# Optimization experiments

Measured on AMD Instinct MI355X. Metric: run time of the kernel, lower is better.

Reference implementation:

```python
import jax, jax.numpy as jnp
import numpy as np
import math

LMAX = 2
NUM_Z = 4
N_NODES = 20000
N_GRAPHS = 5000
N_EDGES = 320000
# irreps as (mul, l, parity)
IR_SH   = [(1, 0, 1), (1, 1, -1), (1, 2, 1)]
IR_ATTR = [(NUM_Z**2, 0, 1), (NUM_Z**2, 1, -1), (NUM_Z**2, 2, 1)]
IR_MID  = [(64, 0, 1), (24, 1, 1), (24, 1, -1), (16, 2, 1), (16, 2, -1)]
IR_OUT  = [(1, 0, -1), (6, 0, 1)]


def _cg(j1, j2, j3, m1, m2, m3):
    if m1 + m2 != m3:
        return 0.0
    f = math.factorial
    pre = math.sqrt((2 * j3 + 1) * f(j3 + j1 - j2) * f(j3 - j1 + j2) * f(j1 + j2 - j3) / f(j1 + j2 + j3 + 1))
    pre *= math.sqrt(f(j3 + m3) * f(j3 - m3) * f(j1 - m1) * f(j1 + m1) * f(j2 - m2) * f(j2 + m2))
    s = 0.0
    for k in range(max(0, j2 - j3 - m1, j1 - j3 + m2), min(j1 + j2 - j3, j1 - m1, j2 + m2) + 1):
        s += (-1) ** k / (f(k) * f(j1 + j2 - j3 - k) * f(j1 - m1 - k) * f(j2 + m2 - k) * f(j3 - j2 + m1 + k) * f(j3 - j1 - m2 + k))
    return pre * s


def _u(l):
    # complex -> real spherical harmonics change of basis, m = -l..l
    U = np.zeros((2 * l + 1, 2 * l + 1), dtype=complex)
    for m in range(-l, l + 1):
        if m > 0:
            U[m + l, -m + l] = 1 / math.sqrt(2)
            U[m + l, m + l] = (-1) ** m / math.sqrt(2)
        elif m == 0:
            U[l, l] = 1.0
        else:
            U[m + l, m + l] = 1j / math.sqrt(2)
            U[m + l, -m + l] = -1j * (-1) ** (-m) / math.sqrt(2)
    return U


def _w3j(l1, l2, l3):
    C = np.zeros((2 * l1 + 1, 2 * l2 + 1, 2 * l3 + 1))
    for m1 in range(-l1, l1 + 1):
        for m2 in range(-l2, l2 + 1):
            m3 = m1 + m2
            if -l3 <= m3 <= l3:
                C[m1 + l1, m2 + l2, m3 + l3] = _cg(l1, l2, l3, m1, m2, m3)
    T = np.einsum('am,bn,co,mno->abc', _u(l1), _u(l2), _u(l3).conj(), C.astype(complex))
    T = T.real if np.abs(T.real).max() >= np.abs(T.imag).max() else T.imag
    return (T / np.linalg.norm(T)).astype(np.float32)  # Frobenius norm 1, e3nn convention


W3J = {(a, b, c): _w3j(a, b, c) for a in range(3) for b in range(3) for c in range(3) if abs(a - b) <= c <= a + b}


def _slices(ir):
    s = [0]
    for m, l, _ in ir:
        s.append(s[-1] + m * (2 * l + 1))
    return s


def _paths(ir1, ir2, iro):
    paths = []
    fan = [0] * len(iro)
    off = 0
    for a, (m1, l1, p1) in enumerate(ir1):
        for b, (m2, l2, p2) in enumerate(ir2):
            for c, (m3, l3, p3) in enumerate(iro):
                if p1 * p2 == p3 and abs(l1 - l2) <= l3 <= l1 + l2:
                    paths.append((a, b, c, off))
                    fan[c] += m1 * m2
                    off += m1 * m2 * m3
    return paths, fan, off


def _fctp(x1, x2, w, ir1, ir2, iro):
    # FullyConnectedTensorProduct: 'uvw' weighted Clebsch-Gordan contraction per path
    s1, s2 = _slices(ir1), _slices(ir2)
    paths, fan, _ = _paths(ir1, ir2, iro)
    E = x1.shape[0]
    out = [jnp.zeros((E, m * (2 * l + 1)), x1.dtype) for m, l, _ in iro]
    for a, b, c, off in paths:
        m1, l1, _ = ir1[a]
        m2, l2, _ = ir2[b]
        m3, l3, _ = iro[c]
        W = w[off:off + m1 * m2 * m3].reshape(m1, m2, m3)
        C = jnp.asarray(W3J[(l1, l2, l3)], x1.dtype)
        xa = x1[:, s1[a]:s1[a + 1]].reshape(E, m1, 2 * l1 + 1)
        xb = x2[:, s2[b]:s2[b + 1]].reshape(E, m2, 2 * l2 + 1)
        alpha = math.sqrt(2 * l3 + 1) / math.sqrt(fan[c])
        y = jnp.einsum('eui,evj,ijk,uvw->ewk', xa, xb, C, W)
        out[c] = out[c] + (alpha * y).reshape(E, -1)
    return jnp.concatenate(out, axis=1)


def _sh(v):
    # component-normalized harmonic polynomials for l=0,1,2 (normalize=False)
    x, y, z = v[:, 0], v[:, 1], v[:, 2]
    r2 = x * x + y * y + z * z
    s3, s15, s5 = math.sqrt(3.0), math.sqrt(15.0), math.sqrt(5.0)
    sh1 = s3 * jnp.stack([y, z, x], axis=1)
    sh2 = jnp.stack([s15 * x * y, s15 * y * z, 0.5 * s5 * (3 * z * z - r2), s15 * x * z, 0.5 * s15 * (x * x - y * y)], axis=1)
    return jnp.concatenate([jnp.ones_like(x)[:, None], sh1, sh2], axis=1)  # [E, 9]


def _forward(pos, w_tp1, w_tp2, z, batch, edge_src, edge_dst):
    E = edge_src.shape[0]
    ev = pos[edge_src] - pos[edge_dst]
    sh = _sh(ev)
    zz = NUM_Z * z[edge_src] + z[edge_dst]
    zzf = jax.nn.one_hot(zz, NUM_Z ** 2, dtype=sh.dtype) * NUM_Z  # [E, 16]
    # 'uvu' TensorProduct of (16x0e) with sh: outer product per l block
    blocks = [(0, 1), (1, 4), (4, 9)]
    edge_attr = jnp.concatenate([(zzf[:, :, None] * sh[:, None, a:b]).reshape(E, -1) for a, b in blocks], axis=1)
    inv_nn = 1.0 / math.sqrt(3.0)  # num_neighbors = 3
    node = jax.ops.segment_sum(sh, edge_dst, num_segments=N_NODES) * inv_nn
    ef = _fctp(node[edge_src], edge_attr, w_tp1, IR_SH, IR_ATTR, IR_MID)
    node = jax.ops.segment_sum(ef, edge_dst, num_segments=N_NODES) * inv_nn
    ef = _fctp(node[edge_src], edge_attr, w_tp2, IR_MID, IR_ATTR, IR_OUT)
    node = jax.ops.segment_sum(ef, edge_dst, num_segments=N_NODES) * inv_nn
    return jax.ops.segment_sum(node, batch, num_segments=N_GRAPHS) * 0.5  # num_nodes = 4


def setup_inputs() -> dict:
    key = jax.random.key(0)
    k = jax.random.split(key, 7)
    _, _, n1 = _paths(IR_SH, IR_ATTR, IR_MID)
    _, _, n2 = _paths(IR_MID, IR_ATTR, IR_OUT)
    return {
        'pos': jax.random.normal(k[0], (N_NODES, 3), jnp.float32),
        'z': jax.random.randint(k[1], (N_NODES,), 0, NUM_Z, jnp.int32),
        'batch': jnp.sort(jax.random.randint(k[2], (N_NODES,), 0, N_GRAPHS, jnp.int32)),
        'edge_src': jax.random.randint(k[3], (N_EDGES,), 0, N_NODES, jnp.int32),
        'edge_dst': jax.random.randint(k[4], (N_EDGES,), 0, N_NODES, jnp.int32),
        'w_tp1': jax.random.normal(k[5], (n1,), jnp.float32),
        'w_tp2': jax.random.normal(k[6], (n2,), jnp.float32),
    }


def reference(pos, z, batch, edge_src, edge_dst, w_tp1, w_tp2):
    return _forward(pos, w_tp1, w_tp2, z, batch, edge_src, edge_dst)
```

## Files before the change

kernel.cpp:

```cpp
#include <hip/hip_runtime.h>


#define N_EDGES   320000
#define NN_NODES  20000
#define NN_GRAPHS 5000

__device__ __forceinline__ void sh_from_vec(float x, float y, float z,
                                            float* B1, float* B2) {
    const float s3   = 1.7320508075688772f;
    const float s15  = 3.8729833462074170f;
    const float s5h  = 1.1180339887498949f;
    const float s15h = 1.9364916731037085f;
    B1[0] = s3 * y; B1[1] = s3 * z; B1[2] = s3 * x;
    float r2 = x * x + y * y + z * z;
    B2[0] = s15 * x * y;
    B2[1] = s15 * y * z;
    B2[2] = s5h * (3.f * z * z - r2);
    B2[3] = s15 * x * z;
    B2[4] = s15h * (x * x - y * y);
}

__global__ __launch_bounds__(256) void k_zero(const float* __restrict__ pos,
                                              int* __restrict__ counts,
                                              float* __restrict__ out,
                                              float4* __restrict__ pos4) {
    int tid = blockIdx.x * blockDim.x + threadIdx.x;
    int stride = gridDim.x * blockDim.x;
    for (int i = tid; i < NN_NODES; i += stride) counts[i] = 0;
    for (int i = tid; i < NN_GRAPHS * 7; i += stride) out[i] = 0.f;
    for (int i = tid; i < NN_NODES; i += stride) {
        float4 p;
        p.x = pos[3 * i]; p.y = pos[3 * i + 1]; p.z = pos[3 * i + 2]; p.w = 0.f;
        pos4[i] = p;
    }
}

__global__ __launch_bounds__(256) void k_hist(const int* __restrict__ edst,
                                              int* __restrict__ counts) {
    int e = blockIdx.x * blockDim.x + threadIdx.x;
    if (e < N_EDGES) atomicAdd(&counts[edst[e]], 1);
}

__global__ __launch_bounds__(1024) void k_scan(const int* __restrict__ counts,
                                               int* __restrict__ start,
                                               int* __restrict__ cursor) {
    __shared__ int sdata[1024];
    __shared__ int carry;
    int tid = threadIdx.x;
    if (tid == 0) carry = 0;
    __syncthreads();
    for (int base = 0; base < NN_NODES; base += 1024) {
        int i = base + tid;
        int v = (i < NN_NODES) ? counts[i] : 0;
        sdata[tid] = v;
        __syncthreads();
        for (int off = 1; off < 1024; off <<= 1) {
            int t = (tid >= off) ? sdata[tid - off] : 0;
            __syncthreads();
            sdata[tid] += t;
            __syncthreads();
        }
        int incl = sdata[tid];
        int c = carry;
        if (i < NN_NODES) {
            int excl = c + incl - v;
            start[i] = excl;
            cursor[i] = excl;
        }
        __syncthreads();
        if (tid == 0) carry = c + sdata[1023];
        __syncthreads();
    }
    if (tid == 0) start[NN_NODES] = carry;
}

__global__ __launch_bounds__(256) void k_fill(const int* __restrict__ esrc,
                                              const int* __restrict__ edst,
                                              const int* __restrict__ zarr,
                                              int* __restrict__ cursor,
                                              int* __restrict__ csr) {
    int e = blockIdx.x * blockDim.x + threadIdx.x;
    if (e >= N_EDGES) return;
    int d = edst[e];
    int s = esrc[e];
    int q = 4 * zarr[s] + zarr[d];
    int p = atomicAdd(&cursor[d], 1);
    csr[p] = s | (q << 16) | ((d & 7) << 20);
}

__global__ __launch_bounds__(256) void k_nodesh(const float4* __restrict__ pos4,
                                                const int* __restrict__ start,
                                                const int* __restrict__ csr,
                                                float* __restrict__ node_sh) {
    int wave = threadIdx.x >> 6;
    int lane = threadIdx.x & 63;
    int n = blockIdx.x * 4 + wave;
    if (n >= NN_NODES) return;
    float4 pd = pos4[n];
    int s0 = start[n], s1 = start[n + 1];
    float acc[9] = {0.f, 0.f, 0.f, 0.f, 0.f, 0.f, 0.f, 0.f, 0.f};
    for (int idx = s0 + lane; idx < s1; idx += 64) {
        int s = csr[idx] & 0xFFFF;
        float4 ps = pos4[s];
        float x = ps.x - pd.x;
        float y = ps.y - pd.y;
        float z = ps.z - pd.z;
        float B1[3], B2[5];
        sh_from_vec(x, y, z, B1, B2);
        acc[0] += 1.f;
        acc[1] += B1[0]; acc[2] += B1[1]; acc[3] += B1[2];
        acc[4] += B2[0]; acc[5] += B2[1]; acc[6] += B2[2];
        acc[7] += B2[3]; acc[8] += B2[4];
    }
#pragma unroll
    for (int off = 32; off > 0; off >>= 1)
#pragma unroll
        for (int i = 0; i < 9; i++) acc[i] += __shfl_down(acc[i], off, 64);
    if (lane == 0) {
        const float inv_nn = 0.57735026918962576f;
#pragma unroll
        for (int i = 0; i < 9; i++) node_sh[n * 12 + i] = acc[i] * inv_nn;
    }
}

__global__ __launch_bounds__(512, 6) void k_mid(const float4* __restrict__ pos4,
                                                const float* __restrict__ node_sh,
                                                const int* __restrict__ start,
                                                const int* __restrict__ csr,
                                                const float* __restrict__ w1,
                                                float* __restrict__ mid) {
    __shared__ float Gl[8 * 816];
    int t = threadIdx.x;
    for (int i = t; i < 8 * 816; i += 512) Gl[i] = 0.f;
    __syncthreads();

    int nbase = blockIdx.x * 8;
    int e0 = start[nbase], e1 = start[nbase + 8];

    const float r3  = 0.57735026918962576f;
    const float r5  = 0.44721359549995794f;
    const float r6  = 0.40824829046386302f;
    const float r10 = 0.31622776601683794f;
    const float s30 = 0.18257418583505536f;
    const float rt3 = 1.7320508075688772f;
    const float c222 = 0.58554004376911990f;
    const float q6 = 0.40824829046386302f;
    const float h6 = 0.20412414523193151f;
    const float h2 = 0.35355339059327376f;
    const float r2c = 0.70710678118654752f;

    for (int idx = e0 + t; idx < e1; idx += 512) {
        int pk = csr[idx];
        int s = pk & 0xFFFF;
        int q = (pk >> 16) & 15;
        int r = (pk >> 20) & 7;
        float4 pd = pos4[nbase + r];
        float4 ps = pos4[s];
        float x = ps.x - pd.x;
        float y = ps.y - pd.y;
        float z = ps.z - pd.z;
        float B1[3], B2[5];
        sh_from_vec(x, y, z, B1, B2);
        const float4 nv0 = *(const float4*)(node_sh + s * 12);
        const float4 nv1 = *(const float4*)(node_sh + s * 12 + 4);
        float a0 = nv0.x;
        float A1[3] = {nv0.y, nv0.z, nv0.w};
        float A2[5] = {nv1.x, nv1.y, nv1.z, nv1.w, node_sh[s * 12 + 8]};
        float* gr = Gl + r * 816 + q * 51;

        atomicAdd(gr + 0, a0);
        atomicAdd(gr + 1, a0 * B1[0] * r3);
        atomicAdd(gr + 2, a0 * B1[1] * r3);
        atomicAdd(gr + 3, a0 * B1[2] * r3);
        atomicAdd(gr + 4, a0 * B2[0] * r5);
        atomicAdd(gr + 5, a0 * B2[1] * r5);
        atomicAdd(gr + 6, a0 * B2[2] * r5);
        atomicAdd(gr + 7, a0 * B2[3] * r5);
        atomicAdd(gr + 8, a0 * B2[4] * r5);
        atomicAdd(gr + 9,  A1[0] * r3);
        atomicAdd(gr + 10, A1[1] * r3);
        atomicAdd(gr + 11, A1[2] * r3);
        atomicAdd(gr + 12, -r3 * (A1[0] * B1[0] + A1[1] * B1[1] + A1[2] * B1[2]));
        atomicAdd(gr + 13, -r6 * (A1[1] * B1[2] - A1[2] * B1[1]));
        atomicAdd(gr + 14, -r6 * (A1[2] * B1[0] - A1[0] * B1[2]));
        atomicAdd(gr + 15, -r6 * (A1[0] * B1[1] - A1[1] * B1[0]));
        atomicAdd(gr + 16, r10 * (A1[0] * B1[2] + A1[2] * B1[0]));
        atomicAdd(gr + 17, r10 * (A1[0] * B1[1] + A1[1] * B1[0]));
        atomicAdd(gr + 18, s30 * (2.f * A1[1] * B1[1] - A1[0] * B1[0] - A1[2] * B1[2]));
        atomicAdd(gr + 19, r10 * (A1[1] * B1[2] + A1[2] * B1[1]));
        atomicAdd(gr + 20, r10 * (A1[2] * B1[2] - A1[0] * B1[0]));
        {
            float Byy = -B2[2] * q6 - B2[4] * r2c;
            float Bzz = 2.f * B2[2] * q6;
            float Bxx = -B2[2] * q6 + B2[4] * r2c;
            float Bxy = B2[0] * r2c;
            float Byz = B2[1] * r2c;
            float Bxz = B2[3] * r2c;
            atomicAdd(gr + 21, -r5 * (Byy * A1[0] + Byz * A1[1] + Bxy * A1[2]));
            atomicAdd(gr + 22, -r5 * (Byz * A1[0] + Bzz * A1[1] + Bxz * A1[2]));
            atomicAdd(gr + 23, -r5 * (Bxy * A1[0] + Bxz * A1[1] + Bxx * A1[2]));
        }
        atomicAdd(gr + 24, -s30 * (B2[1] * A1[0] - B2[3] * A1[2] + 2.f * B2[4] * A1[1]));
        atomicAdd(gr + 25, -s30 * (-B2[0] * A1[0] - rt3 * B2[2] * A1[2] + B2[3] * A1[1] - B2[4] * A1[2]));
        atomicAdd(gr + 26, -s30 * (rt3 * B2[1] * A1[2] - rt3 * B2[3] * A1[0]));
        atomicAdd(gr + 27, -s30 * (B2[0] * A1[2] - B2[1] * A1[1] + rt3 * B2[2] * A1[0] - B2[4] * A1[0]));
        atomicAdd(gr + 28, -s30 * (-2.f * B2[0] * A1[1] + B2[1] * A1[2] + B2[3] * A1[0]));
        atomicAdd(gr + 29, A2[0] * r5);
        atomicAdd(gr + 30, A2[1] * r5);
        atomicAdd(gr + 31, A2[2] * r5);
        atomicAdd(gr + 32, A2[3] * r5);
        atomicAdd(gr + 33, A2[4] * r5);
        {
            float Ayy = -A2[2] * q6 - A2[4] * r2c;
            float Azz = 2.f * A2[2] * q6;
            float Axx = -A2[2] * q6 + A2[4] * r2c;
            float Axy = A2[0] * r2c;
            float Ayz = A2[1] * r2c;
            float Axz = A2[3] * r2c;
            atomicAdd(gr + 34, -r5 * (Ayy * B1[0] + Ayz * B1[1] + Axy * B1[2]));
            atomicAdd(gr + 35, -r5 * (Ayz * B1[0] + Azz * B1[1] + Axz * B1[2]));
            atomicAdd(gr + 36, -r5 * (Axy * B1[0] + Axz * B1[1] + Axx * B1[2]));
        }
        atomicAdd(gr + 37, s30 * (A2[1] * B1[0] - A2[3] * B1[2] + 2.f * A2[4] * B1[1]));
        atomicAdd(gr + 38, s30 * (-A2[0] * B1[0] - rt3 * A2[2] * B1[2] + A2[3] * B1[1] - A2[4] * B1[2]));
        atomicAdd(gr + 39, s30 * (rt3 * A2[1] * B1[2] - rt3 * A2[3] * B1[0]));
        atomicAdd(gr + 40, s30 * (A2[0] * B1[2] - A2[1] * B1[1] + rt3 * A2[2] * B1[0] - A2[4] * B1[0]));
        atomicAdd(gr + 41, s30 * (-2.f * A2[0] * B1[1] + A2[1] * B1[2] + A2[3] * B1[0]));
        atomicAdd(gr + 42, r5 * (A2[0] * B2[0] + A2[1] * B2[1] + A2[2] * B2[2] +
                                 A2[3] * B2[3] + A2[4] * B2[4]));
        atomicAdd(gr + 43, s30 * (-A2[0] * B2[1] + A2[1] * B2[0] +
                                  rt3 * (A2[2] * B2[3] - A2[3] * B2[2]) +
                                  A2[3] * B2[4] - A2[4] * B2[3]));
        atomicAdd(gr + 44, s30 * (-2.f * A2[0] * B2[4] + 2.f * A2[4] * B2[0] -
                                  A2[1] * B2[3] + A2[3] * B2[1]));
        atomicAdd(gr + 45, s30 * (A2[0] * B2[3] - A2[3] * B2[0] +
                                  rt3 * (A2[1] * B2[2] - A2[2] * B2[1]) +
                                  A2[1] * B2[4] - A2[4] * B2[1]));
        atomicAdd(gr + 46, -c222 * (-q6 * (A2[0] * B2[2] + A2[2] * B2[0]) +
                                    h2 * (A2[1] * B2[3] + A2[3] * B2[1])));
        atomicAdd(gr + 47, -c222 * (h6 * (A2[1] * B2[2] + A2[2] * B2[1]) -
                                    h2 * (A2[1] * B2[4] + A2[4] * B2[1]) +
                                    h2 * (A2[0] * B2[3] + A2[3] * B2[0])));
        atomicAdd(gr + 48, -c222 * (q6 * (A2[2] * B2[2] - A2[0] * B2[0] - A2[4] * B2[4]) +
                                    h6 * (A2[1] * B2[1] + A2[3] * B2[3])));
        atomicAdd(gr + 49, -c222 * (h6 * (A2[3] * B2[2] + A2[2] * B2[3]) +
                                    h2 * (A2[3] * B2[4] + A2[4] * B2[3]) +
                                    h2 * (A2[0] * B2[1] + A2[1] * B2[0])));
        atomicAdd(gr + 50, -c222 * (-q6 * (A2[4] * B2[2] + A2[2] * B2[4]) +
                                    h2 * (A2[3] * B2[3] - A2[1] * B2[1])));
    }
    __syncthreads();

    int j = t;
    if (j >= 368) return;
    float acc[8] = {0.f, 0.f, 0.f, 0.f, 0.f, 0.f, 0.f, 0.f};
    if (j < 64) {
        int w = j;
        for (int q = 0; q < 16; q++) {
            float wa = w1[q * 64 + w];
            float wb = w1[2048 + q * 64 + w];
            float wc = w1[5248 + q * 64 + w];
            const float* Gq = Gl + q * 51;
#pragma unroll
            for (int r2 = 0; r2 < 8; r2++) {
                const float* gq = Gq + r2 * 816;
                acc[r2] += gq[0] * wa + gq[12] * wb + gq[42] * wc;
            }
        }
#pragma unroll
        for (int r2 = 0; r2 < 8; r2++)
            mid[(size_t)(nbase + r2) * 368 + j] = 0.33333333333333333f * acc[r2];
    } else if (j < 136) {
        int tt = j - 64, w = tt / 3, k = tt - 3 * w;
        for (int q = 0; q < 16; q++) {
            float wa = w1[3072 + q * 24 + w];
            float wb = w1[6272 + q * 24 + w];
            const float* Gq = Gl + q * 51;
#pragma unroll
            for (int r2 = 0; r2 < 8; r2++) {
                const float* gq = Gq + r2 * 816;
                acc[r2] += gq[13 + k] * wa + gq[43 + k] * wb;
            }
        }
#pragma unroll
        for (int r2 = 0; r2 < 8; r2++)
            mid[(size_t)(nbase + r2) * 368 + j] = 0.70710678118654752f * acc[r2];
    } else if (j < 208) {
        int tt = j - 136, w = tt / 3, k = tt - 3 * w;
        for (int q = 0; q < 16; q++) {
            float wa = w1[1024 + q * 24 + w];
            float wb = w1[1664 + q * 24 + w];
            float wc = w1[3712 + q * 24 + w];
            float wd = w1[4608 + q * 24 + w];
            const float* Gq = Gl + q * 51;
#pragma unroll
            for (int r2 = 0; r2 < 8; r2++) {
                const float* gq = Gq + r2 * 816;
                acc[r2] += gq[1 + k] * wa + gq[9 + k] * wb +
                           gq[21 + k] * wc + gq[34 + k] * wd;
            }
        }
#pragma unroll
        for (int r2 = 0; r2 < 8; r2++)
            mid[(size_t)(nbase + r2) * 368 + j] = 0.5f * acc[r2];
    } else if (j < 288) {
        int tt = j - 208, w = tt / 5, k = tt - 5 * w;
        for (int q = 0; q < 16; q++) {
            float wa = w1[1408 + q * 16 + w];
            float wb = w1[3456 + q * 16 + w];
            float wc = w1[4352 + q * 16 + w];
            float wd = w1[6656 + q * 16 + w];
            const float* Gq = Gl + q * 51;
#pragma unroll
            for (int r2 = 0; r2 < 8; r2++) {
                const float* gq = Gq + r2 * 816;
                acc[r2] += gq[4 + k] * wa + gq[16 + k] * wb +
                           gq[29 + k] * wc + gq[46 + k] * wd;
            }
        }
#pragma unroll
        for (int r2 = 0; r2 < 8; r2++)
            mid[(size_t)(nbase + r2) * 368 + j] = 0.64549722436790280f * acc[r2];
    } else {
        int tt = j - 288, w = tt / 5, k = tt - 5 * w;
        for (int q = 0; q < 16; q++) {
            float wa = w1[4096 + q * 16 + w];
            float wb = w1[4992 + q * 16 + w];
            const float* Gq = Gl + q * 51;
#pragma unroll
            for (int r2 = 0; r2 < 8; r2++) {
                const float* gq = Gq + r2 * 816;
                acc[r2] += gq[24 + k] * wa + gq[37 + k] * wb;
            }
        }
#pragma unroll
        for (int r2 = 0; r2 < 8; r2++)
            mid[(size_t)(nbase + r2) * 368 + j] = 0.91287092917527690f * acc[r2];
    }
}

__global__ __launch_bounds__(1024, 8) void k_out(const float4* __restrict__ pos4,
                                                 const int* __restrict__ batch,
                                                 const int* __restrict__ start,
                                                 const int* __restrict__ csr,
                                                 const float* __restrict__ mid,
                                                 const float* __restrict__ w2,
                                                 float* __restrict__ out) {
    __shared__ float lw2[10624];
    for (int i = threadIdx.x; i < 10624; i += 1024) {
        int src;
        if (i < 4096) {
            int w = i & 3, u = (i >> 2) & 63, q = i >> 8;
            src = (u * 16 + q) * 6 + w;
        } else if (i < 6144) {
            int t2 = i - 4096;
            int w = t2 & 1, u = (t2 >> 1) & 63, q = t2 >> 7;
            src = (u * 16 + q) * 6 + 4 + w;
        } else if (i < 6528) {
            int t2 = i - 6144;
            int u = t2 % 24, q = t2 / 24;
            src = 6144 + u * 16 + q;
        } else if (i < 8064) {
            int t2 = i - 6528;
            int w = t2 & 3, a = t2 >> 2;
            int u = a % 24, q = a / 24;
            src = 6528 + (u * 16 + q) * 6 + w;
        } else if (i < 8832) {
            int t2 = i - 8064;
            int w = t2 & 1, a = t2 >> 1;
            int u = a % 24, q = a / 24;
            src = 6528 + (u * 16 + q) * 6 + 4 + w;
        } else if (i < 9856) {
            int t2 = i - 8832;
            int w = t2 & 3, a = t2 >> 2;
            int u = a & 15, q = a >> 4;
            src = 8832 + (u * 16 + q) * 6 + w;
        } else if (i < 10368) {
            int t2 = i - 9856;
            int w = t2 & 1, a = t2 >> 1;
            int u = a & 15, q = a >> 4;
            src = 8832 + (u * 16 + q) * 6 + 4 + w;
        } else {
            int t2 = i - 10368;
            int u = t2 & 15, q = t2 >> 4;
            src = 10368 + u * 16 + q;
        }
        lw2[i] = w2[src];
    }
    __syncthreads();

    int wave = threadIdx.x >> 6;
    int lane = threadIdx.x & 63;
    int n = blockIdx.x * 16 + wave;
    float4 pd = pos4[n];
    int s0 = start[n], s1 = start[n + 1];

    int offA;
    if (lane < 24)      offA = 64  + 3 * lane;
    else if (lane < 48) offA = 136 + 3 * (lane - 24);
    else                offA = 208 + 5 * (lane - 48);
    const int offB = 288 + 5 * lane;

    float p0[6] = {0.f, 0.f, 0.f, 0.f, 0.f, 0.f};
    float pA[6] = {0.f, 0.f, 0.f, 0.f, 0.f, 0.f};
    float pB = 0.f;

    for (int idx = s0; idx < s1; ++idx) {
        int pk = csr[idx];
        pk = __builtin_amdgcn_readfirstlane(pk);
        int s = pk & 0xFFFF;
        int q = (pk >> 16) & 15;
        const float* mrow = mid + (size_t)s * 368;

        float m  = mrow[lane];
        float a0 = mrow[offA], a1 = mrow[offA + 1], a2 = mrow[offA + 2];
        float a3 = 0.f, a4 = 0.f;
        if (lane >= 48) { a3 = mrow[offA + 3]; a4 = mrow[offA + 4]; }
        float b0 = 0.f, b1 = 0.f, b2 = 0.f, b3 = 0.f, b4 = 0.f;
        if (lane < 16) {
            b0 = mrow[offB];     b1 = mrow[offB + 1]; b2 = mrow[offB + 2];
            b3 = mrow[offB + 3]; b4 = mrow[offB + 4];
        }
        float4 ps = pos4[s];
        float x = ps.x - pd.x;
        float y = ps.y - pd.y;
        float z = ps.z - pd.z;

        float B1[3], B2[5];
        sh_from_vec(x, y, z, B1, B2);

        {
            const float4 wv  = *(const float4*)(lw2 + q * 256 + lane * 4);
            const float2 wv2 = *(const float2*)(lw2 + 4096 + q * 128 + lane * 2);
            p0[0] += m * wv.x;  p0[1] += m * wv.y;
            p0[2] += m * wv.z;  p0[3] += m * wv.w;
            p0[4] += m * wv2.x; p0[5] += m * wv2.y;
        }
        float dd;
        if (lane < 48) dd = a0 * B1[0] + a1 * B1[1] + a2 * B1[2];
        else           dd = a0 * B2[0] + a1 * B2[1] + a2 * B2[2] +
                            a3 * B2[3] + a4 * B2[4];
        if (lane < 24) {
            pA[0] += dd * lw2[6144 + q * 24 + lane];
        } else if (lane < 48) {
            int u = lane - 24;
            const float4 wv  = *(const float4*)(lw2 + 6528 + q * 96 + u * 4);
            const float2 wv2 = *(const float2*)(lw2 + 8064 + q * 48 + u * 2);
            pA[0] += dd * wv.x;  pA[1] += dd * wv.y;
            pA[2] += dd * wv.z;  pA[3] += dd * wv.w;
            pA[4] += dd * wv2.x; pA[5] += dd * wv2.y;
        } else {
            int u = lane - 48;
            const float4 wv  = *(const float4*)(lw2 + 8832 + q * 64 + u * 4);
            const float2 wv2 = *(const float2*)(lw2 + 9856 + q * 32 + u * 2);
            pA[0] += dd * wv.x;  pA[1] += dd * wv.y;
            pA[2] += dd * wv.z;  pA[3] += dd * wv.w;
            pA[4] += dd * wv2.x; pA[5] += dd * wv2.y;
        }
        if (lane < 16) {
            float ddB = b0 * B2[0] + b1 * B2[1] + b2 * B2[2] +
                        b3 * B2[3] + b4 * B2[4];
            pB += ddB * lw2[10368 + q * 16 + lane];
        }
    }

    const float cT0f =  0.02830690f;
    const float cT1f = -0.02635231f;
    const float cT2f = -0.01634300f;
    const float cT3f =  0.01265893f;
    const float cT4f =  0.02041241f;

    float o0 = 0.f;
    float ov[6];
#pragma unroll
    for (int w = 0; w < 6; w++) ov[w] = cT0f * p0[w];
    if (lane < 24) {
        o0 += cT1f * pA[0];
    } else if (lane < 48) {
#pragma unroll
        for (int w = 0; w < 6; w++) ov[w] += cT2f * pA[w];
    } else {
#pragma unroll
        for (int w = 0; w < 6; w++) ov[w] += cT3f * pA[w];
    }
    if (lane < 16) o0 += cT4f * pB;

#pragma unroll
    for (int off = 32; off > 0; off >>= 1) {
        o0 += __shfl_down(o0, off, 64);
#pragma unroll
        for (int w = 0; w < 6; w++) ov[w] += __shfl_down(ov[w], off, 64);
    }
    if (lane == 0) {
        float* og = out + batch[n] * 7;
        atomicAdd(og + 0, o0);
#pragma unroll
        for (int w = 0; w < 6; w++) atomicAdd(og + 1 + w, ov[w]);
    }
}

extern "C" void kernel_launch(void* const* d_in, const int* in_sizes, int n_in,
                              void* d_out, int out_size, void* d_ws, size_t ws_size,
                              hipStream_t stream) {
    const float* pos  = (const float*)d_in[0];
    const int*   z    = (const int*)d_in[1];
    const int*   bat  = (const int*)d_in[2];
    const int*   esrc = (const int*)d_in[3];
    const int*   edst = (const int*)d_in[4];
    const float* w1   = (const float*)d_in[5];
    const float* w2   = (const float*)d_in[6];
    float* out = (float*)d_out;

    int*   wsI = (int*)d_ws;
    float* wsF = (float*)d_ws;
    int* counts = wsI + 0;
    int* start  = wsI + 32768;
    int* cursor = wsI + 65536;
    int* csr    = wsI + 98304;
    float4* pos4   = (float4*)(wsF + 425984);
    float* node_sh = wsF + 524288;
    float* mid     = wsF + 1048576;

    k_zero<<<64, 256, 0, stream>>>(pos, counts, out, pos4);
    k_hist<<<(N_EDGES + 255) / 256, 256, 0, stream>>>(edst, counts);
    k_scan<<<1, 1024, 0, stream>>>(counts, start, cursor);
    k_fill<<<(N_EDGES + 255) / 256, 256, 0, stream>>>(esrc, edst, z, cursor, csr);
    k_nodesh<<<NN_NODES / 4, 256, 0, stream>>>(pos4, start, csr, node_sh);
    k_mid<<<NN_NODES / 8, 512, 0, stream>>>(pos4, node_sh, start, csr, w1, mid);
    k_out<<<NN_NODES / 16, 1024, 0, stream>>>(pos4, bat, start, csr, mid, w2, out);
}
```

Before: 415.9 us.

## Scatter output stage over source-node CSR and use shared atomics in node SH

Builds a second CSR keyed by source node, with destination, species pair and graph id packed per edge. The output kernel now loads each node's mid row once and loops over its outgoing edges, reducing across the wave and issuing global atomics into the graph output for every edge. This replaces the old per-edge gather of 368-float mid rows. The node-SH kernel now handles 16 destination nodes per block and accumulates with shared-memory atomics. The cost is an extra histogram, scan and fill pass, plus a full wave reduction and seven global atomics per edge instead of one set per node.

```diff
diff --git a/kernel.cpp b/kernel.cpp
--- a/kernel.cpp
+++ b/kernel.cpp
@@ -22,11 +22,12 @@
 
 __global__ __launch_bounds__(256) void k_zero(const float* __restrict__ pos,
                                               int* __restrict__ counts,
+                                              int* __restrict__ counts2,
                                               float* __restrict__ out,
                                               float4* __restrict__ pos4) {
     int tid = blockIdx.x * blockDim.x + threadIdx.x;
     int stride = gridDim.x * blockDim.x;
-    for (int i = tid; i < NN_NODES; i += stride) counts[i] = 0;
+    for (int i = tid; i < NN_NODES; i += stride) { counts[i] = 0; counts2[i] = 0; }
     for (int i = tid; i < NN_GRAPHS * 7; i += stride) out[i] = 0.f;
     for (int i = tid; i < NN_NODES; i += stride) {
         float4 p;
@@ -35,43 +36,54 @@
     }
 }
 
-__global__ __launch_bounds__(256) void k_hist(const int* __restrict__ edst,
-                                              int* __restrict__ counts) {
+__global__ __launch_bounds__(256) void k_hist(const int* __restrict__ esrc,
+                                              const int* __restrict__ edst,
+                                              int* __restrict__ counts,
+                                              int* __restrict__ counts2) {
     int e = blockIdx.x * blockDim.x + threadIdx.x;
-    if (e < N_EDGES) atomicAdd(&counts[edst[e]], 1);
-}
-
-__global__ __launch_bounds__(1024) void k_scan(const int* __restrict__ counts,
-                                               int* __restrict__ start,
-                                               int* __restrict__ cursor) {
-    __shared__ int sdata[1024];
-    __shared__ int carry;
+    if (e < N_EDGES) {
+        atomicAdd(&counts[edst[e]], 1);
+        atomicAdd(&counts2[esrc[e]], 1);
+    }
+}
+
+__global__ __launch_bounds__(1024) void k_scan2(const int* __restrict__ counts,
+                                                const int* __restrict__ counts2,
+                                                int* __restrict__ start,
+                                                int* __restrict__ cursor,
+                                                int* __restrict__ start2,
+                                                int* __restrict__ cursor2) {
+    __shared__ int sa[1024];
+    __shared__ int sb[1024];
+    __shared__ int carryA, carryB;
     int tid = threadIdx.x;
-    if (tid == 0) carry = 0;
+    if (tid == 0) { carryA = 0; carryB = 0; }
     __syncthreads();
     for (int base = 0; base < NN_NODES; base += 1024) {
         int i = base + tid;
-        int v = (i < NN_NODES) ? counts[i] : 0;
-        sdata[tid] = v;
+        int va = (i < NN_NODES) ? counts[i] : 0;
+        int vb = (i < NN_NODES) ? counts2[i] : 0;
+        sa[tid] = va; sb[tid] = vb;
         __syncthreads();
         for (int off = 1; off < 1024; off <<= 1) {
-            int t = (tid >= off) ? sdata[tid - off] : 0;
+            int ta = (tid >= off) ? sa[tid - off] : 0;
+            int tb = (tid >= off) ? sb[tid - off] : 0;
             __syncthreads();
-            sdata[tid] += t;
+            sa[tid] += ta; sb[tid] += tb;
             __syncthreads();
         }
-        int incl = sdata[tid];
-        int c = carry;
+        int cA = carryA, cB = carryB;
         if (i < NN_NODES) {
-            int excl = c + incl - v;
-            start[i] = excl;
-            cursor[i] = excl;
+            int ea = cA + sa[tid] - va;
+            int eb = cB + sb[tid] - vb;
+            start[i] = ea;  cursor[i] = ea;
+            start2[i] = eb; cursor2[i] = eb;
         }
         __syncthreads();
-        if (tid == 0) carry = c + sdata[1023];
+        if (tid == 0) { carryA = cA + sa[1023]; carryB = cB + sb[1023]; }
         __syncthreads();
     }
-    if (tid == 0) start[NN_NODES] = carry;
+    if (tid == 0) { start[NN_NODES] = carryA; start2[NN_NODES] = carryB; }
 }
 
 __global__ __launch_bounds__(256) void k_fill(const int* __restrict__ esrc,
@@ -85,41 +97,56 @@
     int s = esrc[e];
     int q = 4 * zarr[s] + zarr[d];
     int p = atomicAdd(&cursor[d], 1);
-    csr[p] = s | (q << 16) | ((d & 7) << 20);
+    csr[p] = s | (q << 16) | ((d & 15) << 20);
+}
+
+__global__ __launch_bounds__(256) void k_fill2(const int* __restrict__ esrc,
+                                               const int* __restrict__ edst,
+                                               const int* __restrict__ zarr,
+                                               const int* __restrict__ batch,
+                                               int* __restrict__ cursor2,
+                                               int* __restrict__ csr) {
+    int e = blockIdx.x * blockDim.x + threadIdx.x;
+    if (e >= N_EDGES) return;
+    int d = edst[e];
+    int s = esrc[e];
+    int q = 4 * zarr[s] + zarr[d];
+    int p = atomicAdd(&cursor2[s], 1);
+    csr[p] = d | (q << 15) | (batch[d] << 19);
 }
 
 __global__ __launch_bounds__(256) void k_nodesh(const float4* __restrict__ pos4,
                                                 const int* __restrict__ start,
                                                 const int* __restrict__ csr,
                                                 float* __restrict__ node_sh) {
-    int wave = threadIdx.x >> 6;
-    int lane = threadIdx.x & 63;
-    int n = blockIdx.x * 4 + wave;
-    if (n >= NN_NODES) return;
-    float4 pd = pos4[n];
-    int s0 = start[n], s1 = start[n + 1];
-    float acc[9] = {0.f, 0.f, 0.f, 0.f, 0.f, 0.f, 0.f, 0.f, 0.f};
-    for (int idx = s0 + lane; idx < s1; idx += 64) {
-        int s = csr[idx] & 0xFFFF;
+    __shared__ float ns[16][12];
+    int t = threadIdx.x;
+    if (t < 192) ns[t / 12][t % 12] = 0.f;
+    __syncthreads();
+    int nbase = blockIdx.x * 16;
+    int e0 = start[nbase], e1 = start[nbase + 16];
+    for (int idx = e0 + t; idx < e1; idx += 256) {
+        int pk = csr[idx];
+        int s = pk & 0xFFFF;
+        int r = (pk >> 20) & 15;
+        float4 pd = pos4[nbase + r];
         float4 ps = pos4[s];
         float x = ps.x - pd.x;
         float y = ps.y - pd.y;
         float z = ps.z - pd.z;
         float B1[3], B2[5];
         sh_from_vec(x, y, z, B1, B2);
-        acc[0] += 1.f;
-        acc[1] += B1[0]; acc[2] += B1[1]; acc[3] += B1[2];
-        acc[4] += B2[0]; acc[5] += B2[1]; acc[6] += B2[2];
-        acc[7] += B2[3]; acc[8] += B2[4];
-    }
-#pragma unroll
-    for (int off = 32; off > 0; off >>= 1)
-#pragma unroll
-        for (int i = 0; i < 9; i++) acc[i] += __shfl_down(acc[i], off, 64);
-    if (lane == 0) {
+        float* nr = &ns[r][0];
+        atomicAdd(nr + 0, 1.f);
+        atomicAdd(nr + 1, B1[0]); atomicAdd(nr + 2, B1[1]); atomicAdd(nr + 3, B1[2]);
+        atomicAdd(nr + 4, B2[0]); atomicAdd(nr + 5, B2[1]); atomicAdd(nr + 6, B2[2]);
+        atomicAdd(nr + 7, B2[3]); atomicAdd(nr + 8, B2[4]);
+    }
+    __syncthreads();
+    if (t < 144) {
+        int r = t / 9, c = t % 9;
         const float inv_nn = 0.57735026918962576f;
-#pragma unroll
-        for (int i = 0; i < 9; i++) node_sh[n * 12 + i] = acc[i] * inv_nn;
+        node_sh[(size_t)(nbase + r) * 12 + c] = ns[r][c] * inv_nn;
     }
 }
 
@@ -340,9 +367,8 @@
 }
 
 __global__ __launch_bounds__(1024, 8) void k_out(const float4* __restrict__ pos4,
-                                                 const int* __restrict__ batch,
-                                                 const int* __restrict__ start,
-                                                 const int* __restrict__ csr,
+                                                 const int* __restrict__ start2,
+                                                 const int* __restrict__ csr2,
                                                  const float* __restrict__ mid,
                                                  const float* __restrict__ w2,
                                                  float* __restrict__ out) {
@@ -392,8 +418,8 @@
     int wave = threadIdx.x >> 6;
     int lane = threadIdx.x & 63;
     int n = blockIdx.x * 16 + wave;
-    float4 pd = pos4[n];
-    int s0 = start[n], s1 = start[n + 1];
+    float4 ps = pos4[n];
+    int s0 = start2[n], s1 = start2[n + 1];
 
     int offA;
     if (lane < 24)      offA = 64  + 3 * lane;
@@ -401,67 +427,15 @@
     else                offA = 208 + 5 * (lane - 48);
     const int offB = 288 + 5 * lane;
 
-    float p0[6] = {0.f, 0.f, 0.f, 0.f, 0.f, 0.f};
-    float pA[6] = {0.f, 0.f, 0.f, 0.f, 0.f, 0.f};
-    float pB = 0.f;
-
-    for (int idx = s0; idx < s1; ++idx) {
-        int pk = csr[idx];
-        pk = __builtin_amdgcn_readfirstlane(pk);
-        int s = pk & 0xFFFF;
-        int q = (pk >> 16) & 15;
-        const float* mrow = mid + (size_t)s * 368;
-
-        float m  = mrow[lane];
-        float a0 = mrow[offA], a1 = mrow[offA + 1], a2 = mrow[offA + 2];
-        float a3 = 0.f, a4 = 0.f;
-        if (lane >= 48) { a3 = mrow[offA + 3]; a4 = mrow[offA + 4]; }
-        float b0 = 0.f, b1 = 0.f, b2 = 0.f, b3 = 0.f, b4 = 0.f;
-        if (lane < 16) {
-            b0 = mrow[offB];     b1 = mrow[offB + 1]; b2 = mrow[offB + 2];
-            b3 = mrow[offB + 3]; b4 = mrow[offB + 4];
-        }
-        float4 ps = pos4[s];
-        float x = ps.x - pd.x;
-        float y = ps.y - pd.y;
-        float z = ps.z - pd.z;
-
-        float B1[3], B2[5];
-        sh_from_vec(x, y, z, B1, B2);
-
-        {
-            const float4 wv  = *(const float4*)(lw2 + q * 256 + lane * 4);
-            const float2 wv2 = *(const float2*)(lw2 + 4096 + q * 128 + lane * 2);
-            p0[0] += m * wv.x;  p0[1] += m * wv.y;
-            p0[2] += m * wv.z;  p0[3] += m * wv.w;
-            p0[4] += m * wv2.x; p0[5] += m * wv2.y;
-        }
-        float dd;
-        if (lane < 48) dd = a0 * B1[0] + a1 * B1[1] + a2 * B1[2];
-        else           dd = a0 * B2[0] + a1 * B2[1] + a2 * B2[2] +
-                            a3 * B2[3] + a4 * B2[4];
-        if (lane < 24) {
-            pA[0] += dd * lw2[6144 + q * 24 + lane];
-        } else if (lane < 48) {
-            int u = lane - 24;
-            const float4 wv  = *(const float4*)(lw2 + 6528 + q * 96 + u * 4);
-            const float2 wv2 = *(const float2*)(lw2 + 8064 + q * 48 + u * 2);
-            pA[0] += dd * wv.x;  pA[1] += dd * wv.y;
-            pA[2] += dd * wv.z;  pA[3] += dd * wv.w;
-            pA[4] += dd * wv2.x; pA[5] += dd * wv2.y;
-        } else {
-            int u = lane - 48;
-            const float4 wv  = *(const float4*)(lw2 + 8832 + q * 64 + u * 4);
-            const float2 wv2 = *(const float2*)(lw2 + 9856 + q * 32 + u * 2);
-            pA[0] += dd * wv.x;  pA[1] += dd * wv.y;
-            pA[2] += dd * wv.z;  pA[3] += dd * wv.w;
-            pA[4] += dd * wv2.x; pA[5] += dd * wv2.y;
-        }
-        if (lane < 16) {
-            float ddB = b0 * B2[0] + b1 * B2[1] + b2 * B2[2] +
-                        b3 * B2[3] + b4 * B2[4];
-            pB += ddB * lw2[10368 + q * 16 + lane];
-        }
+    const float* mrow = mid + (size_t)n * 368;
+    float m  = mrow[lane];
+    float a0 = mrow[offA], a1 = mrow[offA + 1], a2 = mrow[offA + 2];
+    float a3 = 0.f, a4 = 0.f;
+    if (lane >= 48) { a3 = mrow[offA + 3]; a4 = mrow[offA + 4]; }
+    float b0 = 0.f, b1 = 0.f, b2 = 0.f, b3 = 0.f, b4 = 0.f;
+    if (lane < 16) {
+        b0 = mrow[offB];     b1 = mrow[offB + 1]; b2 = mrow[offB + 2];
+        b3 = mrow[offB + 3]; b4 = mrow[offB + 4];
     }
 
     const float cT0f =  0.02830690f;
@@ -470,32 +444,65 @@
     const float cT3f =  0.01265893f;
     const float cT4f =  0.02041241f;
 
-    float o0 = 0.f;
-    float ov[6];
-#pragma unroll
-    for (int w = 0; w < 6; w++) ov[w] = cT0f * p0[w];
-    if (lane < 24) {
-        o0 += cT1f * pA[0];
-    } else if (lane < 48) {
-#pragma unroll
-        for (int w = 0; w < 6; w++) ov[w] += cT2f * pA[w];
-    } else {
-#pragma unroll
-        for (int w = 0; w < 6; w++) ov[w] += cT3f * pA[w];
-    }
-    if (lane < 16) o0 += cT4f * pB;
-
-#pragma unroll
-    for (int off = 32; off > 0; off >>= 1) {
-        o0 += __shfl_down(o0, off, 64);
-#pragma unroll
-        for (int w = 0; w < 6; w++) ov[w] += __shfl_down(ov[w], off, 64);
-    }
-    if (lane == 0) {
-        float* og = out + batch[n] * 7;
-        atomicAdd(og + 0, o0);
-#pragma unroll
-        for (int w = 0; w < 6; w++) atomicAdd(og + 1 + w, ov[w]);
+    for (int idx = s0; idx < s1; ++idx) {
+        int pk = csr2[idx];
+        pk = __builtin_amdgcn_readfirstlane(pk);
+        int d = pk & 0x7FFF;
+        int q = (pk >> 15) & 15;
+        int b = (pk >> 19) & 0x1FFF;
+        float4 pd = pos4[d];
+        float x = ps.x - pd.x;
+        float y = ps.y - pd.y;
+        float z = ps.z - pd.z;
+
+        float B1[3], B2[5];
+        sh_from_vec(x, y, z, B1, B2);
+
+        float o[7];
+        {
+            const float4 wv  = *(const float4*)(lw2 + q * 256 + lane * 4);
+            const float2 wv2 = *(const float2*)(lw2 + 4096 + q * 128 + lane * 2);
+            o[1] = cT0f * m * wv.x;  o[2] = cT0f * m * wv.y;
+            o[3] = cT0f * m * wv.z;  o[4] = cT0f * m * wv.w;
+            o[5] = cT0f * m * wv2.x; o[6] = cT0f * m * wv2.y;
+        }
+        float dd;
+        if (lane < 48) dd = a0 * B1[0] + a1 * B1[1] + a2 * B1[2];
+        else           dd = a0 * B2[0] + a1 * B2[1] + a2 * B2[2] +
+                            a3 * B2[3] + a4 * B2[4];
+        o[0] = 0.f;
+        if (lane < 24) {
+            o[0] = cT1f * dd * lw2[6144 + q * 24 + lane];
+        } else if (lane < 48) {
+            int u = lane - 24;
+            const float4 wv  = *(const float4*)(lw2 + 6528 + q * 96 + u * 4);
+            const float2 wv2 = *(const float2*)(lw2 + 8064 + q * 48 + u * 2);
+            o[1] += cT2f * dd * wv.x;  o[2] += cT2f * dd * wv.y;
+            o[3] += cT2f * dd * wv.z;  o[4] += cT2f * dd * wv.w;
+            o[5] += cT2f * dd * wv2.x; o[6] += cT2f * dd * wv2.y;
+        } else {
+            int u = lane - 48;
+            const float4 wv  = *(const float4*)(lw2 + 8832 + q * 64 + u * 4);
+            const float2 wv2 = *(const float2*)(lw2 + 9856 + q * 32 + u * 2);
+            o[1] += cT3f * dd * wv.x;  o[2] += cT3f * dd * wv.y;
+            o[3] += cT3f * dd * wv.z;  o[4] += cT3f * dd * wv.w;
+            o[5] += cT3f * dd * wv2.x; o[6] += cT3f * dd * wv2.y;
+        }
+        if (lane < 16) {
+            float ddB = b0 * B2[0] + b1 * B2[1] + b2 * B2[2] +
+                        b3 * B2[3] + b4 * B2[4];
+            o[0] += cT4f * ddB * lw2[10368 + q * 16 + lane];
+        }
+
+#pragma unroll
+        for (int off = 32; off > 0; off >>= 1)
+#pragma unroll
+            for (int i = 0; i < 7; i++) o[i] += __shfl_down(o[i], off, 64);
+        if (lane == 0) {
+            float* og = out + b * 7;
+#pragma unroll
+            for (int i = 0; i < 7; i++) atomicAdd(og + i, o[i]);
+        }
     }
 }
 
@@ -513,19 +520,23 @@
 
     int*   wsI = (int*)d_ws;
     float* wsF = (float*)d_ws;
-    int* counts = wsI + 0;
-    int* start  = wsI + 32768;
-    int* cursor = wsI + 65536;
-    int* csr    = wsI + 98304;
+    int* counts  = wsI + 0;
+    int* start   = wsI + 32768;
+    int* cursor  = wsI + 65536;
+    int* csr     = wsI + 98304;
     float4* pos4   = (float4*)(wsF + 425984);
     float* node_sh = wsF + 524288;
+    int* counts2 = wsI + 770048;
+    int* start2  = wsI + 790528;
+    int* cursor2 = wsI + 811008;
     float* mid     = wsF + 1048576;
 
-    k_zero<<<64, 256, 0, stream>>>(pos, counts, out, pos4);
-    k_hist<<<(N_EDGES + 255) / 256, 256, 0, stream>>>(edst, counts);
-    k_scan<<<1, 1024, 0, stream>>>(counts, start, cursor);
+    k_zero<<<64, 256, 0, stream>>>(pos, counts, counts2, out, pos4);
+    k_hist<<<(N_EDGES + 255) / 256, 256, 0, stream>>>(esrc, edst, counts, counts2);
+    k_scan2<<<1, 1024, 0, stream>>>(counts, counts2, start, cursor, start2, cursor2);
     k_fill<<<(N_EDGES + 255) / 256, 256, 0, stream>>>(esrc, edst, z, cursor, csr);
-    k_nodesh<<<NN_NODES / 4, 256, 0, stream>>>(pos4, start, csr, node_sh);
+    k_nodesh<<<NN_NODES / 16, 256, 0, stream>>>(pos4, start, csr, node_sh);
     k_mid<<<NN_NODES / 8, 512, 0, stream>>>(pos4, node_sh, start, csr, w1, mid);
-    k_out<<<NN_NODES / 16, 1024, 0, stream>>>(pos4, bat, start, csr, mid, w2, out);
-}
+    k_fill2<<<(N_EDGES + 255) / 256, 256, 0, stream>>>(esrc, edst, z, bat, cursor2, csr);
+    k_out<<<NN_NODES / 16, 1024, 0, stream>>>(pos4, start2, csr, mid, w2, out);
+}
```

New measurement: 565.0 us. 35.8% more time.
